# Performance work log

Measured on AMD Instinct MI355X. Metric: run time of the kernel, lower is better.

## Reference

```python
import jax, jax.numpy as jnp
import numpy as np

N, E, W, G = 100000, 625000, 128, 64  # nodes, edges, width, num graphs
EPS = 1e-5


def setup_inputs() -> dict:
    key = jax.random.key(0)
    ks = jax.random.split(key, 8)
    x = jax.random.normal(ks[0], (N, W), jnp.float32)
    edge_index = jax.random.randint(ks[1], (2, E), 0, N, dtype=jnp.int32)
    edge_weight = jax.random.uniform(ks[2], (E,), jnp.float32)
    batch_map = jnp.sort(jax.random.randint(ks[3], (N,), 0, G, dtype=jnp.int32))
    s = 1.0 / np.sqrt(W)
    return {
        "x": x,
        "edge_index": edge_index,
        "edge_weight": edge_weight,
        "batch_map": batch_map,
        "gn_weight": jnp.ones((W,), jnp.float32),
        "gn_bias": jnp.zeros((W,), jnp.float32),
        "gn_mean_scale": jnp.ones((W,), jnp.float32),
        "W_rel1": jax.random.normal(ks[4], (W, W), jnp.float32) * s,
        "b_rel1": jnp.zeros((W,), jnp.float32),
        "W_root1": jax.random.normal(ks[5], (W, W), jnp.float32) * s,
        "W_rel2": jax.random.normal(ks[6], (W, W), jnp.float32) * s,
        "b_rel2": jnp.zeros((W,), jnp.float32),
        "W_root2": jax.random.normal(ks[7], (W, W), jnp.float32) * s,
    }


def _graph_norm(x, batch, weight, bias, mean_scale):
    # per-graph mean / var keyed on batch_map (PyG GraphNorm)
    cnt = jax.ops.segment_sum(jnp.ones((x.shape[0], 1), x.dtype), batch, num_segments=G)
    mean = jax.ops.segment_sum(x, batch, num_segments=G) / cnt
    out = x - mean_scale * mean[batch]
    var = jax.ops.segment_sum(out * out, batch, num_segments=G) / cnt
    std = jnp.sqrt(var + EPS)
    return weight * out / std[batch] + bias


def _graph_conv(x, src, dst, ew, W_rel, b_rel, W_root):
    # out_i = W_rel @ sum_{j->i} e_ji * x_j + b_rel + W_root @ x_i
    msg = x[src] * ew[:, None]                       # [E, W] gather
    agg = jax.ops.segment_sum(msg, dst, num_segments=x.shape[0])  # scatter-add
    return agg @ W_rel.T + b_rel + x @ W_root.T


def reference(x, edge_index, edge_weight, batch_map,
              gn_weight, gn_bias, gn_mean_scale,
              W_rel1, b_rel1, W_root1, W_rel2, b_rel2, W_root2):
    src, dst = edge_index[0], edge_index[1]
    xx = _graph_norm(x, batch_map, gn_weight, gn_bias, gn_mean_scale)
    xx = _graph_conv(xx, src, dst, edge_weight, W_rel1, b_rel1, W_root1)
    xx = jnp.where(xx >= 0, xx, 0.1 * xx)            # LeakyReLU(0.1)
    xx = _graph_conv(xx, src, dst, edge_weight, W_rel2, b_rel2, W_root2)
    return x + xx
```

## Files before the change

### kernel.cpp

```cpp
#include <hip/hip_runtime.h>
#include <hip/hip_bf16.h>

#define WW 128
#define GG 64
#define GN_EPS 1e-5f
#define SCAN_B 1024

typedef __attribute__((ext_vector_type(8))) short short8;
typedef __attribute__((ext_vector_type(4))) float floatx4;

__device__ inline float bf2f(__hip_bfloat16 h) { return __bfloat162float(h); }

__global__ __launch_bounds__(128) void stats_kernel(
    const float* __restrict__ x, const int* __restrict__ batch, int N,
    float* __restrict__ gsum, float* __restrict__ gsumsq, float* __restrict__ gcnt)
{
    int w = threadIdx.x;
    int row0 = blockIdx.x * 64;
    int row1 = min(row0 + 64, N);
    float s = 0.f, ss = 0.f;
    int cur = batch[row0];
    int cnt = 0;
    auto flush = [&]() {
        atomicAdd(&gsum[cur * WW + w], s);
        atomicAdd(&gsumsq[cur * WW + w], ss);
        if (w == 0) atomicAdd(&gcnt[cur], (float)cnt);
        s = 0.f; ss = 0.f; cnt = 0;
    };
    int i = row0;
    for (; i + 4 <= row1; i += 4) {
        int g0 = batch[i + 0], g1 = batch[i + 1], g2 = batch[i + 2], g3 = batch[i + 3];
        float v0 = x[(size_t)(i + 0) * WW + w];
        float v1 = x[(size_t)(i + 1) * WW + w];
        float v2 = x[(size_t)(i + 2) * WW + w];
        float v3 = x[(size_t)(i + 3) * WW + w];
        if (g0 != cur) { flush(); cur = g0; }
        s += v0; ss += v0 * v0; ++cnt;
        if (g1 != cur) { flush(); cur = g1; }
        s += v1; ss += v1 * v1; ++cnt;
        if (g2 != cur) { flush(); cur = g2; }
        s += v2; ss += v2 * v2; ++cnt;
        if (g3 != cur) { flush(); cur = g3; }
        s += v3; ss += v3 * v3; ++cnt;
    }
    for (; i < row1; ++i) {
        int g = batch[i];
        float v = x[(size_t)i * WW + w];
        if (g != cur) { flush(); cur = g; }
        s += v; ss += v * v; ++cnt;
    }
    flush();
}

__global__ __launch_bounds__(256) void finalize_kernel(
    const float* __restrict__ gsum, const float* __restrict__ gsumsq,
    const float* __restrict__ gcnt,
    const float* __restrict__ wgt, const float* __restrict__ bias,
    const float* __restrict__ ms,
    float* __restrict__ scalev, float* __restrict__ shiftv)
{
    int idx = blockIdx.x * blockDim.x + threadIdx.x;
    if (idx >= GG * WW) return;
    int g = idx >> 7, w = idx & (WW - 1);
    float cnt = gcnt[g];
    float inv = cnt > 0.f ? 1.f / cnt : 0.f;
    float mean = gsum[idx] * inv;
    float msw = ms[w];
    float var = gsumsq[idx] * inv - mean * mean * msw * (2.f - msw);
    var = fmaxf(var, 0.f);
    float sc = wgt[w] * rsqrtf(var + GN_EPS);
    scalev[idx] = sc;
    shiftv[idx] = bias[w] - sc * msw * mean;
}

__global__ __launch_bounds__(256) void normalize_kernel(
    const float* __restrict__ x, const int* __restrict__ batch,
    const float* __restrict__ scalev, const float* __restrict__ shiftv,
    __hip_bfloat16* __restrict__ xn, int N)
{
    size_t tid = (size_t)blockIdx.x * blockDim.x + threadIdx.x;
    if (tid >= (size_t)N * (WW / 4)) return;
    int row = (int)(tid >> 5);
    int c4 = (int)(tid & 31) * 4;
    int g = batch[row];
    float4 v = *(const float4*)(x + (size_t)row * WW + c4);
    float4 sc = *(const float4*)(scalev + (size_t)g * WW + c4);
    float4 sh = *(const float4*)(shiftv + (size_t)g * WW + c4);
    __hip_bfloat162 o0, o1;
    o0.x = __float2bfloat16(sc.x * v.x + sh.x);
    o0.y = __float2bfloat16(sc.y * v.y + sh.y);
    o1.x = __float2bfloat16(sc.z * v.z + sh.z);
    o1.y = __float2bfloat16(sc.w * v.w + sh.w);
    union { __hip_bfloat162 h[2]; uint2 u; } pk;
    pk.h[0] = o0; pk.h[1] = o1;
    *(uint2*)(xn + (size_t)row * WW + c4) = pk.u;
}

__global__ __launch_bounds__(256) void cvt_w_kernel(
    const float* __restrict__ w0, const float* __restrict__ w1,
    const float* __restrict__ w2, const float* __restrict__ w3,
    __hip_bfloat16* __restrict__ dst)
{
    int idx = blockIdx.x * blockDim.x + threadIdx.x;
    int m = idx >> 14;
    int o = idx & 16383;
    const float* src = (m == 0) ? w0 : (m == 1) ? w1 : (m == 2) ? w2 : w3;
    dst[idx] = __float2bfloat16(src[o]);
}

__global__ __launch_bounds__(256) void hist_kernel(
    const int* __restrict__ ei, int E, int* __restrict__ deg)
{
    int e = blockIdx.x * 256 + threadIdx.x;
    if (e < E) atomicAdd(&deg[ei[(size_t)E + e]], 1);
}

__global__ __launch_bounds__(SCAN_B) void scan_blocks(
    const int* __restrict__ deg, int N, int* __restrict__ off, int* __restrict__ bsum)
{
    __shared__ int s[SCAN_B];
    int t = threadIdx.x;
    int i = blockIdx.x * SCAN_B + t;
    int v = (i < N) ? deg[i] : 0;
    s[t] = v; __syncthreads();
    for (int d = 1; d < SCAN_B; d <<= 1) {
        int tmp = (t >= d) ? s[t - d] : 0;
        __syncthreads();
        s[t] += tmp;
        __syncthreads();
    }
    if (i < N) off[i] = s[t] - v;
    if (t == SCAN_B - 1) bsum[blockIdx.x] = s[t];
}

__global__ __launch_bounds__(256) void scan_partials(int* __restrict__ bsum, int P)
{
    __shared__ int s[256];
    int t = threadIdx.x;
    int v = (t < P) ? bsum[t] : 0;
    s[t] = v; __syncthreads();
    for (int d = 1; d < 256; d <<= 1) {
        int tmp = (t >= d) ? s[t - d] : 0;
        __syncthreads();
        s[t] += tmp;
        __syncthreads();
    }
    if (t < P) bsum[t] = s[t] - v;
}

__global__ __launch_bounds__(SCAN_B) void add_offsets(
    int* __restrict__ off, const int* __restrict__ bsum, int N)
{
    int i = blockIdx.x * SCAN_B + threadIdx.x;
    if (i < N) off[i] += bsum[blockIdx.x];
}

__global__ __launch_bounds__(256) void place_kernel(
    const int* __restrict__ ei, const float* __restrict__ ew,
    const int* __restrict__ off, int* __restrict__ cursor,
    int2* __restrict__ ebuf, int E)
{
    int base = blockIdx.x * 1024 + threadIdx.x;
    int dstv[4], srcv[4];
    float wv[4];
    int slot[4];
#pragma unroll
    for (int i = 0; i < 4; ++i) {
        int e = base + i * 256;
        dstv[i] = (e < E) ? ei[(size_t)E + e] : -1;
    }
#pragma unroll
    for (int i = 0; i < 4; ++i) {
        int e = base + i * 256;
        if (e < E) { srcv[i] = ei[e]; wv[i] = ew[e]; }
    }
#pragma unroll
    for (int i = 0; i < 4; ++i)
        if (dstv[i] >= 0) slot[i] = off[dstv[i]] + atomicAdd(&cursor[dstv[i]], 1);
#pragma unroll
    for (int i = 0; i < 4; ++i)
        if (dstv[i] >= 0) ebuf[slot[i]] = make_int2(srcv[i], __float_as_int(wv[i]));
}

__global__ __launch_bounds__(256) void gather_kernel(
    const __hip_bfloat16* __restrict__ feat, const int2* __restrict__ ebuf,
    const int* __restrict__ off, const int* __restrict__ deg,
    __hip_bfloat16* __restrict__ aggbf, int N)
{
    int wave = threadIdx.x >> 6;
    int lane = threadIdx.x & 63;
    int node = blockIdx.x * 4 + wave;
    if (node >= N) return;
    int start = off[node];
    int d = deg[node];
    const __hip_bfloat162* f2 = (const __hip_bfloat162*)feat;

    float ax0 = 0.f, ay0 = 0.f, ax1 = 0.f, ay1 = 0.f;
    float ax2 = 0.f, ay2 = 0.f, ax3 = 0.f, ay3 = 0.f;
    int last = start + d - 1;
    for (int k = start; k <= last; k += 4) {
        int i1 = min(k + 1, last);
        int i2 = min(k + 2, last);
        int i3 = min(k + 3, last);
        int2 p0 = ebuf[k];
        int2 p1 = ebuf[i1];
        int2 p2 = ebuf[i2];
        int2 p3 = ebuf[i3];
        __hip_bfloat162 v0 = f2[(size_t)p0.x * 64 + lane];
        __hip_bfloat162 v1 = f2[(size_t)p1.x * 64 + lane];
        __hip_bfloat162 v2 = f2[(size_t)p2.x * 64 + lane];
        __hip_bfloat162 v3 = f2[(size_t)p3.x * 64 + lane];
        float w0 = __int_as_float(p0.y);
        float w1 = (k + 1 <= last) ? __int_as_float(p1.y) : 0.f;
        float w2 = (k + 2 <= last) ? __int_as_float(p2.y) : 0.f;
        float w3 = (k + 3 <= last) ? __int_as_float(p3.y) : 0.f;
        ax0 += w0 * bf2f(v0.x); ay0 += w0 * bf2f(v0.y);
        ax1 += w1 * bf2f(v1.x); ay1 += w1 * bf2f(v1.y);
        ax2 += w2 * bf2f(v2.x); ay2 += w2 * bf2f(v2.y);
        ax3 += w3 * bf2f(v3.x); ay3 += w3 * bf2f(v3.y);
    }
    float ax = (ax0 + ax1) + (ax2 + ax3);
    float ay = (ay0 + ay1) + (ay2 + ay3);

    __hip_bfloat162 o;
    o.x = __float2bfloat16(ax);
    o.y = __float2bfloat16(ay);
    ((__hip_bfloat162*)(aggbf + (size_t)node * WW))[lane] = o;
}

template <bool OUT_BF16>
__global__ __launch_bounds__(256, 4) void gemm_kernel(
    const __hip_bfloat16* __restrict__ A1, const __hip_bfloat16* __restrict__ A2,
    const __hip_bfloat16* __restrict__ Wrel, const __hip_bfloat16* __restrict__ Wroot,
    const float* __restrict__ bias, const float* __restrict__ resid,
    void* __restrict__ outv, int N, int leaky, int ntiles)
{
    __shared__ __hip_bfloat16 smem[2][2 * 32 * 128];
    int wave = threadIdx.x >> 6;
    int lane = threadIdx.x & 63;
    int q = lane >> 4;
    int r16 = lane & 15;

    auto stage = [&](int tile, int buf) {
#pragma unroll
        for (int s = 0; s < 4; ++s) {
            int t = wave * 4 + s;
            const __hip_bfloat16* Asel = (t < 8) ? A1 : A2;
            int t8 = t & 7;
            int rloc = t8 * 4 + (lane >> 4);
            int c = (lane & 15) ^ (rloc & 15);
            int grow = tile * 32 + rloc; if (grow >= N) grow = N - 1;
            const __hip_bfloat16* g = Asel + (size_t)grow * WW + c * 8;
            __hip_bfloat16* l = &smem[buf][(t >> 3) * 4096 + t8 * 512];
            __builtin_amdgcn_global_load_lds(
                (const __attribute__((address_space(1))) void*)g,
                (__attribute__((address_space(3))) void*)l, 16, 0, 0);
        }
    };

    stage(blockIdx.x, 0);

    short8 wf[8][2];
#pragma unroll
    for (int kc = 0; kc < 8; ++kc) {
        const __hip_bfloat16* Wsel = (kc < 4) ? Wrel : Wroot;
        int koff = (kc & 3) * 32 + q * 8;
#pragma unroll
        for (int tt = 0; tt < 2; ++tt) {
            int col = (wave * 2 + tt) * 16 + r16;
            wf[kc][tt] = *(const short8*)(Wsel + ((size_t)col * WW + koff));
        }
    }
    float bcol[2];
#pragma unroll
    for (int tt = 0; tt < 2; ++tt) bcol[tt] = bias[(wave * 2 + tt) * 16 + r16];

    __syncthreads();

    int cur = 0;
    for (int tile = blockIdx.x; tile < ntiles; tile += gridDim.x) {
        int nxt = tile + gridDim.x;
        if (nxt < ntiles) stage(nxt, cur ^ 1);

        floatx4 acc[2][2];
#pragma unroll
        for (int r = 0; r < 2; ++r)
#pragma unroll
            for (int tt = 0; tt < 2; ++tt) acc[r][tt] = (floatx4){0.f, 0.f, 0.f, 0.f};

#pragma unroll
        for (int kc = 0; kc < 8; ++kc) {
            int m = kc >> 2;
            short8 af[2];
#pragma unroll
            for (int r = 0; r < 2; ++r) {
                int row = r * 16 + r16;
                int slot = ((kc & 3) * 4 + q) ^ r16;
                af[r] = *(const short8*)(&smem[cur][m * 4096 + row * 128 + slot * 8]);
            }
#pragma unroll
            for (int r = 0; r < 2; ++r) {
                acc[r][0] = __builtin_amdgcn_mfma_f32_16x16x32_bf16(af[r], wf[kc][0], acc[r][0], 0, 0, 0);
                acc[r][1] = __builtin_amdgcn_mfma_f32_16x16x32_bf16(af[r], wf[kc][1], acc[r][1], 0, 0, 0);
            }
        }

        int rb = tile * 32;
#pragma unroll
        for (int tt = 0; tt < 2; ++tt) {
            int col = (wave * 2 + tt) * 16 + r16;
#pragma unroll
            for (int r = 0; r < 2; ++r)
#pragma unroll
                for (int rr = 0; rr < 4; ++rr) {
                    int row = rb + r * 16 + q * 4 + rr;
                    if (row < N) {
                        float v = acc[r][tt][rr] + bcol[tt];
                        if (leaky) v = v >= 0.f ? v : 0.1f * v;
                        if (resid) v += resid[(size_t)row * WW + col];
                        if (OUT_BF16)
                            ((__hip_bfloat16*)outv)[(size_t)row * WW + col] = __float2bfloat16(v);
                        else
                            ((float*)outv)[(size_t)row * WW + col] = v;
                    }
                }
        }

        __syncthreads();
        cur ^= 1;
    }
}

extern "C" void kernel_launch(void* const* d_in, const int* in_sizes, int n_in,
                              void* d_out, int out_size, void* d_ws, size_t ws_size,
                              hipStream_t stream) {
    const float* x      = (const float*)d_in[0];
    const int*   ei     = (const int*)d_in[1];
    const float* ew     = (const float*)d_in[2];
    const int*   batch  = (const int*)d_in[3];
    const float* gnw    = (const float*)d_in[4];
    const float* gnb    = (const float*)d_in[5];
    const float* gnm    = (const float*)d_in[6];
    const float* Wrel1  = (const float*)d_in[7];
    const float* brel1  = (const float*)d_in[8];
    const float* Wroot1 = (const float*)d_in[9];
    const float* Wrel2  = (const float*)d_in[10];
    const float* brel2  = (const float*)d_in[11];
    const float* Wroot2 = (const float*)d_in[12];

    int N = in_sizes[0] / WW;
    int E = in_sizes[1] / 2;
    int P = (N + SCAN_B - 1) / SCAN_B;
    int ntiles = (N + 31) / 32;
    int ggrid = (ntiles + 2) / 3;

    __hip_bfloat16* aggbf = (__hip_bfloat16*)d_ws;
    __hip_bfloat16* xn = aggbf + (size_t)N * WW;
    __hip_bfloat16* y1 = xn + (size_t)N * WW;
    __hip_bfloat16* Wb = y1 + (size_t)N * WW;
    int2* ebuf   = (int2*)(Wb + 4 * WW * WW);
    int*  deg    = (int*)(ebuf + E);
    int*  cursor = deg + N;
    float* gsum   = (float*)(cursor + N);
    float* gsumsq = gsum + GG * WW;
    float* gcnt   = gsumsq + GG * WW;
    float* scalev = gcnt + GG;
    float* shiftv = scalev + GG * WW;
    int*  off    = (int*)(shiftv + GG * WW);
    int*  bsum   = off + N;

    hipMemsetAsync(deg, 0, ((size_t)2 * N + 2 * GG * WW + GG) * sizeof(int), stream);

    hist_kernel<<<(E + 255) / 256, 256, 0, stream>>>(ei, E, deg);
    scan_blocks<<<P, SCAN_B, 0, stream>>>(deg, N, off, bsum);
    scan_partials<<<1, 256, 0, stream>>>(bsum, P);
    add_offsets<<<P, SCAN_B, 0, stream>>>(off, bsum, N);
    place_kernel<<<(E + 1023) / 1024, 256, 0, stream>>>(ei, ew, off, cursor, ebuf, E);

    cvt_w_kernel<<<(4 * WW * WW) / 256, 256, 0, stream>>>(Wrel1, Wroot1, Wrel2, Wroot2, Wb);
    stats_kernel<<<(N + 63) / 64, 128, 0, stream>>>(x, batch, N, gsum, gsumsq, gcnt);
    finalize_kernel<<<(GG * WW + 255) / 256, 256, 0, stream>>>(
        gsum, gsumsq, gcnt, gnw, gnb, gnm, scalev, shiftv);
    normalize_kernel<<<(int)(((size_t)N * (WW / 4) + 255) / 256), 256, 0, stream>>>(
        x, batch, scalev, shiftv, xn, N);

    gather_kernel<<<(N + 3) / 4, 256, 0, stream>>>(xn, ebuf, off, deg, aggbf, N);
    gemm_kernel<true><<<ggrid, 256, 0, stream>>>(
        aggbf, xn, Wb, Wb + WW * WW, brel1, nullptr, y1, N, 1, ntiles);

    gather_kernel<<<(N + 3) / 4, 256, 0, stream>>>(y1, ebuf, off, deg, aggbf, N);
    gemm_kernel<false><<<ggrid, 256, 0, stream>>>(
        aggbf, y1, Wb + 2 * WW * WW, Wb + 3 * WW * WW, brel2, x, d_out, N, 0, ntiles);
}
```

Baseline: 363.6 us.

## Fuse neighbor gather into GEMM kernel, aggregating directly into LDS

Replaces the separate gather and GEMM kernels with one fused kernel per layer. Each block aggregates the weighted neighbor features for its 32 nodes straight into shared memory, using 8 threads per node with 16-byte loads, and then runs the MFMA GEMM from there. This removes the bf16 aggregate round trip through global memory and two kernel launches. Output columns are remapped so the epilogue writes paired bf16/float2 values. The cost is a non-persistent grid with no double buffering, so GEMM work is not overlapped with the next tile's loads, and high-degree nodes can imbalance a block.

```diff
diff --git a/kernel.cpp b/kernel.cpp
--- a/kernel.cpp
+++ b/kernel.cpp
@@ -10,6 +10,13 @@
 typedef __attribute__((ext_vector_type(4))) float floatx4;
 
 __device__ inline float bf2f(__hip_bfloat16 h) { return __bfloat162float(h); }
+__device__ inline float bfbits2f(short v) {
+    return __uint_as_float(((unsigned)(unsigned short)v) << 16);
+}
+__device__ inline short f2bfbits(float f) {
+    __hip_bfloat16 h = __float2bfloat16(f);
+    return *reinterpret_cast<short*>(&h);
+}
 
 __global__ __launch_bounds__(128) void stats_kernel(
     const float* __restrict__ x, const int* __restrict__ batch, int N,
@@ -182,83 +189,75 @@
         if (dstv[i] >= 0) ebuf[slot[i]] = make_int2(srcv[i], __float_as_int(wv[i]));
 }
 
-__global__ __launch_bounds__(256) void gather_kernel(
-    const __hip_bfloat16* __restrict__ feat, const int2* __restrict__ ebuf,
-    const int* __restrict__ off, const int* __restrict__ deg,
-    __hip_bfloat16* __restrict__ aggbf, int N)
-{
-    int wave = threadIdx.x >> 6;
-    int lane = threadIdx.x & 63;
-    int node = blockIdx.x * 4 + wave;
-    if (node >= N) return;
-    int start = off[node];
-    int d = deg[node];
-    const __hip_bfloat162* f2 = (const __hip_bfloat162*)feat;
-
-    float ax0 = 0.f, ay0 = 0.f, ax1 = 0.f, ay1 = 0.f;
-    float ax2 = 0.f, ay2 = 0.f, ax3 = 0.f, ay3 = 0.f;
+template <bool OUT_BF16>
+__global__ __launch_bounds__(256, 4) void fused_kernel(
+    const __hip_bfloat16* __restrict__ X,
+    const int2* __restrict__ ebuf, const int* __restrict__ off,
+    const int* __restrict__ deg,
+    const __hip_bfloat16* __restrict__ Wrel, const __hip_bfloat16* __restrict__ Wroot,
+    const float* __restrict__ bias, const float* __restrict__ resid,
+    void* __restrict__ outv, int N, int leaky)
+{
+    __shared__ __hip_bfloat16 smem[2 * 32 * 128];
+    int tid = threadIdx.x;
+    int wave = tid >> 6, lane = tid & 63;
+    int q = lane >> 4, r16 = lane & 15;
+    int rb = blockIdx.x * 32;
+
+#pragma unroll
+    for (int s = 0; s < 2; ++s) {
+        int t = wave * 2 + s;
+        int rloc = t * 4 + (lane >> 4);
+        int c = (lane & 15) ^ (rloc & 15);
+        int grow = rb + rloc; if (grow >= N) grow = N - 1;
+        const __hip_bfloat16* g = X + (size_t)grow * WW + c * 8;
+        __hip_bfloat16* l = smem + 4096 + t * 512;
+        __builtin_amdgcn_global_load_lds(
+            (const __attribute__((address_space(1))) void*)g,
+            (__attribute__((address_space(3))) void*)l, 16, 0, 0);
+    }
+
+    int node = rb + (tid >> 3);
+    int nc = node < N ? node : N - 1;
+    int start = off[nc];
+    int d = (node < N) ? deg[nc] : 0;
+    int sub = tid & 7;
+    float a16[16];
+#pragma unroll
+    for (int j = 0; j < 16; ++j) a16[j] = 0.f;
     int last = start + d - 1;
-    for (int k = start; k <= last; k += 4) {
+    for (int k = start; k <= last; k += 2) {
         int i1 = min(k + 1, last);
-        int i2 = min(k + 2, last);
-        int i3 = min(k + 3, last);
         int2 p0 = ebuf[k];
         int2 p1 = ebuf[i1];
-        int2 p2 = ebuf[i2];
-        int2 p3 = ebuf[i3];
-        __hip_bfloat162 v0 = f2[(size_t)p0.x * 64 + lane];
-        __hip_bfloat162 v1 = f2[(size_t)p1.x * 64 + lane];
-        __hip_bfloat162 v2 = f2[(size_t)p2.x * 64 + lane];
-        __hip_bfloat162 v3 = f2[(size_t)p3.x * 64 + lane];
+        const __hip_bfloat16* r0 = X + (size_t)p0.x * WW + sub * 16;
+        const __hip_bfloat16* r1 = X + (size_t)p1.x * WW + sub * 16;
+        short8 a0 = *(const short8*)(r0);
+        short8 b0 = *(const short8*)(r0 + 8);
+        short8 a1 = *(const short8*)(r1);
+        short8 b1 = *(const short8*)(r1 + 8);
         float w0 = __int_as_float(p0.y);
         float w1 = (k + 1 <= last) ? __int_as_float(p1.y) : 0.f;
-        float w2 = (k + 2 <= last) ? __int_as_float(p2.y) : 0.f;
-        float w3 = (k + 3 <= last) ? __int_as_float(p3.y) : 0.f;
-        ax0 += w0 * bf2f(v0.x); ay0 += w0 * bf2f(v0.y);
-        ax1 += w1 * bf2f(v1.x); ay1 += w1 * bf2f(v1.y);
-        ax2 += w2 * bf2f(v2.x); ay2 += w2 * bf2f(v2.y);
-        ax3 += w3 * bf2f(v3.x); ay3 += w3 * bf2f(v3.y);
-    }
-    float ax = (ax0 + ax1) + (ax2 + ax3);
-    float ay = (ay0 + ay1) + (ay2 + ay3);
-
-    __hip_bfloat162 o;
-    o.x = __float2bfloat16(ax);
-    o.y = __float2bfloat16(ay);
-    ((__hip_bfloat162*)(aggbf + (size_t)node * WW))[lane] = o;
-}
-
-template <bool OUT_BF16>
-__global__ __launch_bounds__(256, 4) void gemm_kernel(
-    const __hip_bfloat16* __restrict__ A1, const __hip_bfloat16* __restrict__ A2,
-    const __hip_bfloat16* __restrict__ Wrel, const __hip_bfloat16* __restrict__ Wroot,
-    const float* __restrict__ bias, const float* __restrict__ resid,
-    void* __restrict__ outv, int N, int leaky, int ntiles)
-{
-    __shared__ __hip_bfloat16 smem[2][2 * 32 * 128];
-    int wave = threadIdx.x >> 6;
-    int lane = threadIdx.x & 63;
-    int q = lane >> 4;
-    int r16 = lane & 15;
-
-    auto stage = [&](int tile, int buf) {
-#pragma unroll
-        for (int s = 0; s < 4; ++s) {
-            int t = wave * 4 + s;
-            const __hip_bfloat16* Asel = (t < 8) ? A1 : A2;
-            int t8 = t & 7;
-            int rloc = t8 * 4 + (lane >> 4);
-            int c = (lane & 15) ^ (rloc & 15);
-            int grow = tile * 32 + rloc; if (grow >= N) grow = N - 1;
-            const __hip_bfloat16* g = Asel + (size_t)grow * WW + c * 8;
-            __hip_bfloat16* l = &smem[buf][(t >> 3) * 4096 + t8 * 512];
-            __builtin_amdgcn_global_load_lds(
-                (const __attribute__((address_space(1))) void*)g,
-                (__attribute__((address_space(3))) void*)l, 16, 0, 0);
-        }
-    };
-
-    stage(blockIdx.x, 0);
+#pragma unroll
+        for (int j = 0; j < 8; ++j) {
+            a16[j]     += w0 * bfbits2f(a0[j]) + w1 * bfbits2f(a1[j]);
+            a16[8 + j] += w0 * bfbits2f(b0[j]) + w1 * bfbits2f(b1[j]);
+        }
+    }
+
+    {
+        int r = tid >> 3;
+        short8 pk0, pk1;
+#pragma unroll
+        for (int j = 0; j < 8; ++j) {
+            pk0[j] = f2bfbits(a16[j]);
+            pk1[j] = f2bfbits(a16[8 + j]);
+        }
+        int s0 = (2 * sub)     ^ (r & 15);
+        int s1 = (2 * sub + 1) ^ (r & 15);
+        *(short8*)(smem + r * 128 + s0 * 8) = pk0;
+        *(short8*)(smem + r * 128 + s1 * 8) = pk1;
+    }
 
     short8 wf[8][2];
 #pragma unroll
@@ -267,68 +266,66 @@
         int koff = (kc & 3) * 32 + q * 8;
 #pragma unroll
         for (int tt = 0; tt < 2; ++tt) {
-            int col = (wave * 2 + tt) * 16 + r16;
+            int col = wave * 32 + 2 * r16 + tt;
             wf[kc][tt] = *(const short8*)(Wsel + ((size_t)col * WW + koff));
         }
     }
     float bcol[2];
 #pragma unroll
-    for (int tt = 0; tt < 2; ++tt) bcol[tt] = bias[(wave * 2 + tt) * 16 + r16];
+    for (int tt = 0; tt < 2; ++tt) bcol[tt] = bias[wave * 32 + 2 * r16 + tt];
 
     __syncthreads();
 
-    int cur = 0;
-    for (int tile = blockIdx.x; tile < ntiles; tile += gridDim.x) {
-        int nxt = tile + gridDim.x;
-        if (nxt < ntiles) stage(nxt, cur ^ 1);
-
-        floatx4 acc[2][2];
-#pragma unroll
-        for (int r = 0; r < 2; ++r)
-#pragma unroll
-            for (int tt = 0; tt < 2; ++tt) acc[r][tt] = (floatx4){0.f, 0.f, 0.f, 0.f};
-
-#pragma unroll
-        for (int kc = 0; kc < 8; ++kc) {
-            int m = kc >> 2;
-            short8 af[2];
-#pragma unroll
-            for (int r = 0; r < 2; ++r) {
-                int row = r * 16 + r16;
-                int slot = ((kc & 3) * 4 + q) ^ r16;
-                af[r] = *(const short8*)(&smem[cur][m * 4096 + row * 128 + slot * 8]);
+    floatx4 acc[2][2];
+#pragma unroll
+    for (int r = 0; r < 2; ++r)
+#pragma unroll
+        for (int tt = 0; tt < 2; ++tt) acc[r][tt] = (floatx4){0.f, 0.f, 0.f, 0.f};
+
+#pragma unroll
+    for (int kc = 0; kc < 8; ++kc) {
+        int m = kc >> 2;
+        short8 af[2];
+#pragma unroll
+        for (int r = 0; r < 2; ++r) {
+            int row = r * 16 + r16;
+            int slot = ((kc & 3) * 4 + q) ^ r16;
+            af[r] = *(const short8*)(&smem[m * 4096 + row * 128 + slot * 8]);
+        }
+#pragma unroll
+        for (int r = 0; r < 2; ++r) {
+            acc[r][0] = __builtin_amdgcn_mfma_f32_16x16x32_bf16(af[r], wf[kc][0], acc[r][0], 0, 0, 0);
+            acc[r][1] = __builtin_amdgcn_mfma_f32_16x16x32_bf16(af[r], wf[kc][1], acc[r][1], 0, 0, 0);
+        }
+    }
+
+    int colb = wave * 32 + 2 * r16;
+#pragma unroll
+    for (int r = 0; r < 2; ++r)
+#pragma unroll
+        for (int rr = 0; rr < 4; ++rr) {
+            int row = rb + r * 16 + q * 4 + rr;
+            if (row < N) {
+                float v0 = acc[r][0][rr] + bcol[0];
+                float v1 = acc[r][1][rr] + bcol[1];
+                if (leaky) {
+                    v0 = v0 >= 0.f ? v0 : 0.1f * v0;
+                    v1 = v1 >= 0.f ? v1 : 0.1f * v1;
+                }
+                if (OUT_BF16) {
+                    __hip_bfloat162 o;
+                    o.x = __float2bfloat16(v0);
+                    o.y = __float2bfloat16(v1);
+                    *(__hip_bfloat162*)((__hip_bfloat16*)outv + (size_t)row * WW + colb) = o;
+                } else {
+                    float2 rv = *(const float2*)(resid + (size_t)row * WW + colb);
+                    float2 o;
+                    o.x = v0 + rv.x;
+                    o.y = v1 + rv.y;
+                    *(float2*)((float*)outv + (size_t)row * WW + colb) = o;
+                }
             }
-#pragma unroll
-            for (int r = 0; r < 2; ++r) {
-                acc[r][0] = __builtin_amdgcn_mfma_f32_16x16x32_bf16(af[r], wf[kc][0], acc[r][0], 0, 0, 0);
-                acc[r][1] = __builtin_amdgcn_mfma_f32_16x16x32_bf16(af[r], wf[kc][1], acc[r][1], 0, 0, 0);
-            }
-        }
-
-        int rb = tile * 32;
-#pragma unroll
-        for (int tt = 0; tt < 2; ++tt) {
-            int col = (wave * 2 + tt) * 16 + r16;
-#pragma unroll
-            for (int r = 0; r < 2; ++r)
-#pragma unroll
-                for (int rr = 0; rr < 4; ++rr) {
-                    int row = rb + r * 16 + q * 4 + rr;
-                    if (row < N) {
-                        float v = acc[r][tt][rr] + bcol[tt];
-                        if (leaky) v = v >= 0.f ? v : 0.1f * v;
-                        if (resid) v += resid[(size_t)row * WW + col];
-                        if (OUT_BF16)
-                            ((__hip_bfloat16*)outv)[(size_t)row * WW + col] = __float2bfloat16(v);
-                        else
-                            ((float*)outv)[(size_t)row * WW + col] = v;
-                    }
-                }
-        }
-
-        __syncthreads();
-        cur ^= 1;
-    }
+        }
 }
 
 extern "C" void kernel_launch(void* const* d_in, const int* in_sizes, int n_in,
@@ -352,10 +349,8 @@
     int E = in_sizes[1] / 2;
     int P = (N + SCAN_B - 1) / SCAN_B;
     int ntiles = (N + 31) / 32;
-    int ggrid = (ntiles + 2) / 3;
-
-    __hip_bfloat16* aggbf = (__hip_bfloat16*)d_ws;
-    __hip_bfloat16* xn = aggbf + (size_t)N * WW;
+
+    __hip_bfloat16* xn = (__hip_bfloat16*)d_ws;
     __hip_bfloat16* y1 = xn + (size_t)N * WW;
     __hip_bfloat16* Wb = y1 + (size_t)N * WW;
     int2* ebuf   = (int2*)(Wb + 4 * WW * WW);
@@ -384,11 +379,9 @@
     normalize_kernel<<<(int)(((size_t)N * (WW / 4) + 255) / 256), 256, 0, stream>>>(
         x, batch, scalev, shiftv, xn, N);
 
-    gather_kernel<<<(N + 3) / 4, 256, 0, stream>>>(xn, ebuf, off, deg, aggbf, N);
-    gemm_kernel<true><<<ggrid, 256, 0, stream>>>(
-        aggbf, xn, Wb, Wb + WW * WW, brel1, nullptr, y1, N, 1, ntiles);
-
-    gather_kernel<<<(N + 3) / 4, 256, 0, stream>>>(y1, ebuf, off, deg, aggbf, N);
-    gemm_kernel<false><<<ggrid, 256, 0, stream>>>(
-        aggbf, y1, Wb + 2 * WW * WW, Wb + 3 * WW * WW, brel2, x, d_out, N, 0, ntiles);
-}
+    fused_kernel<true><<<ntiles, 256, 0, stream>>>(
+        xn, ebuf, off, deg, Wb, Wb + WW * WW, brel1, nullptr, y1, N, 1);
+
+    fused_kernel<false><<<ntiles, 256, 0, stream>>>(
+        y1, ebuf, off, deg, Wb + 2 * WW * WW, Wb + 3 * WW * WW, brel2, x, d_out, N, 0);
+}
```

Result: faster. 327.5 us (-9.9%).
